# Kernel tuning notes

Measured on AMD Instinct MI355X. Metric: run time of the kernel, lower is better.

## Reference

```python
import jax, jax.numpy as jnp
import numpy as np

B, T, D_IN, H, L, K = 2048, 96, 64, 256, 2, 20


def setup_inputs() -> dict:
    key = jax.random.key(0)
    ks = jax.random.split(key, 16)
    s = 0.05
    b_ih0 = (jax.random.normal(ks[6], (4 * H,)) * s).at[H:2 * H].set(1.0)
    b_hh0 = (jax.random.normal(ks[7], (4 * H,)) * s).at[H:2 * H].set(1.0)
    b_ih1 = (jax.random.normal(ks[8], (4 * H,)) * s).at[H:2 * H].set(1.0)
    b_hh1 = (jax.random.normal(ks[9], (4 * H,)) * s).at[H:2 * H].set(1.0)
    return {
        "train_batch": jax.random.normal(ks[0], (B, T, D_IN), jnp.float32),
        "labels_batch": jax.random.uniform(ks[1], (B, T), jnp.float32),
        "W_ih0": jax.random.normal(ks[2], (4 * H, D_IN)) * s,
        "W_hh0": jax.random.normal(ks[3], (4 * H, H)) * s,
        "W_ih1": jax.random.normal(ks[4], (4 * H, H)) * s,
        "W_hh1": jax.random.normal(ks[5], (4 * H, H)) * s,
        "b_ih0": b_ih0, "b_hh0": b_hh0, "b_ih1": b_ih1, "b_hh1": b_hh1,
        "W_pb": jax.random.normal(ks[10], (1, H * L)) * s,
        "b_pb": jax.random.normal(ks[11], (1,)) * s,
        "W_pg": jax.random.normal(ks[12], (K, H * L)) * s,
        "b_pg": jax.random.normal(ks[13], (K,)) * s,
    }


def _lstm_cell(x, h, c, Wi, Wh, bi, bh):
    z = x @ Wi.T + h @ Wh.T + bi + bh  # [B, 4H]
    i, f, g, o = jnp.split(z, 4, axis=1)
    c2 = jax.nn.sigmoid(f) * c + jax.nn.sigmoid(i) * jnp.tanh(g)
    h2 = jax.nn.sigmoid(o) * jnp.tanh(c2)
    return h2, c2


def _crps_loss(beta0, gamma, y):
    # beta0: [B,1], gamma: [B,K] (both positive via softplus), y: [B]
    k = gamma.shape[1]
    inv_k = 1.0 / k
    # spline quadratic coefficients beta (per knot)
    prev = jnp.concatenate([beta0, gamma[:, :-1]], axis=1)
    b = (gamma - prev) * (0.5 * k)          # (gamma - prev) / (2*sigma)
    b = b - jnp.pad(b, ((0, 0), (1, 0)))[:, :-1]
    b_last = gamma[:, -1] - jnp.sum(b[:, :-1], axis=1)
    b = jnp.concatenate([b[:, :-1], b_last[:, None]], axis=1)  # [B,K]
    ksi_cum = jnp.cumsum(jnp.full_like(gamma, inv_k), axis=1)  # [B,K]
    ksi = jnp.pad(ksi_cum, ((0, 0), (1, 0)))[:, :-1]           # left knots
    # spline CDF value at each interior knot: F(ksi_cum_i)
    kn = jnp.maximum(ksi_cum[:, :, None] - ksi[:, None, :], 0.0)  # [B,K,K]
    F = ksi_cum * beta0 + jnp.sum(kn * kn * b[:, None, :], axis=-1)  # [B,K]
    knots = jnp.pad(F, ((0, 0), (1, 0)))[:, :-1]  # F at left knot of each segment
    diff = y[:, None] - knots                     # [B,K]
    al = diff > 0                                  # active segments
    alf = al.astype(b.dtype)
    A = jnp.sum(alf * b, axis=1)
    Bc = beta0[:, 0] - 2.0 * jnp.sum(alf * b * ksi, axis=1)
    C = -y + jnp.sum(alf * b * ksi * ksi, axis=1)
    disc = Bc * Bc - 4.0 * A * C
    neg_disc = disc < 0
    A_zero = A == 0
    quad_sel = (~A_zero) & (~neg_disc)
    # fallback: alpha = left knot of segment with min |diff|
    amin = jnp.argmin(jnp.abs(diff), axis=1)
    alpha_knot = jnp.take_along_axis(ksi, amin[:, None], axis=1)[:, 0]
    denB = jnp.where(Bc == 0, 1.0, Bc)
    alpha_lin = -C / denB
    disc_safe = jnp.where(quad_sel, disc, 1.0)
    denA = jnp.where(quad_sel, 2.0 * A, 1.0)
    alpha_quad = (-Bc + jnp.sqrt(disc_safe)) / denA
    alpha = jnp.where(quad_sel, alpha_quad,
                      jnp.where(A_zero, alpha_lin, alpha_knot))
    crps1 = -y * (1.0 - 2.0 * alpha)
    crps2 = beta0[:, 0] * (1.0 / 3.0 - alpha * alpha)
    crps3 = jnp.sum(b / 6.0 * (1.0 - ksi) ** 4, axis=1)
    crps4 = jnp.sum(alf * (2.0 / 3.0) * b * (alpha[:, None] - ksi) ** 3, axis=1)
    return jnp.mean(crps1 + crps2 + crps3 - crps4)


def reference(train_batch, labels_batch, W_ih0, W_hh0, W_ih1, W_hh1,
              b_ih0, b_hh0, b_ih1, b_hh1, W_pb, b_pb, W_pg, b_pg):
    xs = jnp.transpose(train_batch, (1, 0, 2))  # [T,B,D]
    ys = labels_batch.T                          # [T,B]
    bsz = train_batch.shape[0]
    h0 = jnp.zeros((bsz, H), train_batch.dtype)
    init = (h0, h0, h0, h0)

    def step(carry, xy):
        h0_, c0_, h1_, c1_ = carry
        x, y = xy
        h0n, c0n = _lstm_cell(x, h0_, c0_, W_ih0, W_hh0, b_ih0, b_hh0)
        h1n, c1n = _lstm_cell(h0n, h1_, c1_, W_ih1, W_hh1, b_ih1, b_hh1)
        # torch: hidden[L,B,H].permute(1,2,0).reshape(B, H*L)
        hp = jnp.stack([h0n, h1n], axis=-1).reshape(x.shape[0], H * L)
        beta0 = jax.nn.softplus(hp @ W_pb.T + b_pb)  # [B,1]
        gamma = jax.nn.softplus(hp @ W_pg.T + b_pg)  # [B,K]
        return (h0n, c0n, h1n, c1n), _crps_loss(beta0, gamma, y)

    _, losses = jax.lax.scan(step, init, (xs, ys))
    return jnp.sum(losses)
```

## Files before the change

### kernel.cpp

```cpp
#include <hip/hip_runtime.h>


typedef __attribute__((ext_vector_type(8))) short short8v;
typedef __attribute__((ext_vector_type(4))) float f32x4;

#define HBUF 524288
#define GSTRIDE 32768

static __device__ __forceinline__ unsigned short f2bf(float f) {
  unsigned int u = __float_as_uint(f);
  u += 0x7fffu + ((u >> 16) & 1u);
  return (unsigned short)(u >> 16);
}
static __device__ __forceinline__ float sigf(float x) { return 1.f / (1.f + __expf(-x)); }
static __device__ __forceinline__ float tanhfast(float x) {
  float xc = fminf(fmaxf(x, -15.f), 15.f);
  float e = __expf(2.f * xc);
  return (e - 1.f) / (e + 1.f);
}
static __device__ __forceinline__ float softplusf(float x) {
  float e = __expf(-fabsf(x));
  float l = __logf(1.f + e);
  return (x > 0.f) ? x + l : l;
}

__global__ void prep_kernel(const float* __restrict__ Wih0, const float* __restrict__ Whh0,
                            const float* __restrict__ Wih1, const float* __restrict__ Whh1,
                            const float* __restrict__ bih0, const float* __restrict__ bhh0,
                            const float* __restrict__ bih1, const float* __restrict__ bhh1,
                            const float* __restrict__ Wpb,  const float* __restrict__ Wpg,
                            unsigned short* __restrict__ W0, unsigned short* __restrict__ W1,
                            unsigned short* __restrict__ Wp,
                            float* __restrict__ bias0, float* __restrict__ bias1) {
  int i = blockIdx.x * 256 + threadIdx.x;
  if (i < 327680) {
    int s = i / 20480, rem = i % 20480;
    int g = rem / 5120, rem2 = rem % 5120;
    int kk = rem2 >> 9, lane = (rem2 >> 3) & 63, e = rem2 & 7;
    int n = g * 256 + s * 16 + (lane & 15);
    int k = kk * 32 + (lane >> 4) * 8 + e;
    float v = (k < 64) ? Wih0[n * 64 + k] : Whh0[n * 256 + (k - 64)];
    W0[i] = f2bf(v);
    return;
  }
  i -= 327680;
  if (i < 524288) {
    int s = i >> 15, rem = i & 32767;
    int g = rem >> 13, rem2 = rem & 8191;
    int kk = rem2 >> 9, lane = (rem2 >> 3) & 63, e = rem2 & 7;
    int n = g * 256 + s * 16 + (lane & 15);
    int k = kk * 32 + (lane >> 4) * 8 + e;
    float v = (k < 256) ? Wih1[n * 256 + k] : Whh1[n * 256 + (k - 256)];
    W1[i] = f2bf(v);
    return;
  }
  i -= 524288;
  if (i < 16384) {
    int nt = i >> 13, rem = i & 8191;
    int kk = rem >> 9, lane = (rem >> 3) & 63, e = rem & 7;
    int o = nt * 16 + (lane & 15);
    int k = kk * 32 + (lane >> 4) * 8 + e;
    int c = (k < 256) ? (2 * k) : (2 * (k - 256) + 1);
    float v = (o == 0) ? Wpb[c] : (o <= 20 ? Wpg[(o - 1) * 512 + c] : 0.f);
    Wp[i] = f2bf(v);
    return;
  }
  i -= 16384;
  if (i < 1024) { bias0[i] = bih0[i] + bhh0[i]; return; }
  i -= 1024;
  if (i < 1024) { bias1[i] = bih1[i] + bhh1[i]; return; }
}

__global__ __launch_bounds__(512, 2) void lstm_crps_kernel(
    const float* __restrict__ X,
    const float* __restrict__ Y,
    const unsigned short* __restrict__ W0f,
    const unsigned short* __restrict__ W1f,
    const unsigned short* __restrict__ WpF,
    const float* __restrict__ bias0, const float* __restrict__ bias1,
    const float* __restrict__ bpb, const float* __restrict__ bpg,
    unsigned short* __restrict__ H0, unsigned short* __restrict__ H1,
    int* __restrict__ flags,
    float* __restrict__ out) {
  __shared__ __align__(16) unsigned short WL0[20480];
  __shared__ __align__(16) unsigned short WL1[32768];
  __shared__ __align__(16) unsigned short WpL[16384];
  __shared__ float PJ[8][22];
  __shared__ float bpgs[20];
  __shared__ float CB[8][24], KN[8][24];

  const int tid = threadIdx.x;
  const int w  = tid >> 6;
  const int l  = tid & 63;
  const int lr = l & 15;
  const int lg = l >> 4;
  const int bid = blockIdx.x;
  const int grp = (bid & 7) * 2 + ((bid >> 3) & 1);
  const int s   = bid >> 4;

  {
    const int4* src0 = (const int4*)(W0f + s * 20480);
    int4* dst0 = (int4*)WL0;
    for (int i = tid; i < 2560; i += 512) dst0[i] = src0[i];
    const int4* src1 = (const int4*)(W1f + s * 32768);
    int4* dst1 = (int4*)WL1;
    for (int i = tid; i < 4096; i += 512) dst1[i] = src1[i];
    const int4* srcp = (const int4*)WpF;
    int4* dstp = (int4*)WpL;
    for (int i = tid; i < 2048; i += 512) dstp[i] = srcp[i];
    if (tid < 20) bpgs[tid] = bpg[tid];
  }

  float bz0[4], bz1[4];
#pragma unroll
  for (int g = 0; g < 4; ++g) {
    int n = g * 256 + 16 * s + lr;
    bz0[g] = bias0[n];
    bz1[g] = bias1[n];
  }
  float c0s[4] = {}, c1s[4] = {};
  float lossacc = 0.f;
  const float bpbv = bpb[0];

  const int myrow = grp * 128 + w * 16 + lr;
  const float* xrowp = X + (size_t)myrow * 96 * 64 + lg * 8;

  __syncthreads();

  for (int it = 0; it <= 96; ++it) {
    const int tA = it - 1;

    short8v h0f[8], h1f[8];
    if (it >= 1) {
      const unsigned short* hp = H0 + (size_t)(tA & 3) * HBUF + (size_t)myrow * 256 + lg * 8;
#pragma unroll
      for (int kk = 0; kk < 8; ++kk) h0f[kk] = *(const short8v*)(hp + kk * 32);
    }
    if (it >= 2) {
      const unsigned short* hp = H1 + (size_t)(it & 1) * HBUF + (size_t)myrow * 256 + lg * 8;
#pragma unroll
      for (int kk = 0; kk < 8; ++kk) h1f[kk] = *(const short8v*)(hp + kk * 32);
    }
    float4 xa0, xa1, xb0, xb1;
    if (it < 96) {
      const float* xp = xrowp + (size_t)it * 64;
      xa0 = *(const float4*)xp;        xa1 = *(const float4*)(xp + 4);
      xb0 = *(const float4*)(xp + 32); xb1 = *(const float4*)(xp + 36);
    }
    float yv = 0.f;
    if (it >= 1 && tid < 8) yv = Y[(size_t)(grp * 128 + 8 * s + tid) * 96 + tA];

    f32x4 acc[4];

    if (it >= 1) {
#pragma unroll
      for (int g = 0; g < 4; ++g) { f32x4 z = {0.f, 0.f, 0.f, 0.f}; acc[g] = z; }
#pragma unroll
      for (int kk = 0; kk < 8; ++kk)
#pragma unroll
        for (int g = 0; g < 4; ++g) {
          short8v b = *(const short8v*)&WL1[((g * 16 + kk) * 64 + l) * 8];
          acc[g] = __builtin_amdgcn_mfma_f32_16x16x32_bf16(h0f[kk], b, acc[g], 0, 0, 0);
        }
      if (it >= 2) {
#pragma unroll
        for (int kk = 0; kk < 8; ++kk)
#pragma unroll
          for (int g = 0; g < 4; ++g) {
            short8v b = *(const short8v*)&WL1[((g * 16 + 8 + kk) * 64 + l) * 8];
            acc[g] = __builtin_amdgcn_mfma_f32_16x16x32_bf16(h1f[kk], b, acc[g], 0, 0, 0);
          }
      }
      unsigned short* h1c = H1 + (size_t)(tA & 1) * HBUF + grp * GSTRIDE;
#pragma unroll
      for (int r = 0; r < 4; ++r) {
        int rowl = w * 16 + lg * 4 + r;
        float cn = sigf(acc[1][r] + bz1[1]) * c1s[r]
                 + sigf(acc[0][r] + bz1[0]) * tanhfast(acc[2][r] + bz1[2]);
        c1s[r] = cn;
        float hn = sigf(acc[3][r] + bz1[3]) * tanhfast(cn);
        h1c[rowl * 256 + 16 * s + lr] = f2bf(hn);
      }
    }

    if (it < 96) {
#pragma unroll
      for (int g = 0; g < 4; ++g) { f32x4 z = {0.f, 0.f, 0.f, 0.f}; acc[g] = z; }
      {
        short8v a0;
        a0[0] = (short)f2bf(xa0.x); a0[1] = (short)f2bf(xa0.y);
        a0[2] = (short)f2bf(xa0.z); a0[3] = (short)f2bf(xa0.w);
        a0[4] = (short)f2bf(xa1.x); a0[5] = (short)f2bf(xa1.y);
        a0[6] = (short)f2bf(xa1.z); a0[7] = (short)f2bf(xa1.w);
#pragma unroll
        for (int g = 0; g < 4; ++g) {
          short8v b = *(const short8v*)&WL0[((g * 10 + 0) * 64 + l) * 8];
          acc[g] = __builtin_amdgcn_mfma_f32_16x16x32_bf16(a0, b, acc[g], 0, 0, 0);
        }
        short8v a1;
        a1[0] = (short)f2bf(xb0.x); a1[1] = (short)f2bf(xb0.y);
        a1[2] = (short)f2bf(xb0.z); a1[3] = (short)f2bf(xb0.w);
        a1[4] = (short)f2bf(xb1.x); a1[5] = (short)f2bf(xb1.y);
        a1[6] = (short)f2bf(xb1.z); a1[7] = (short)f2bf(xb1.w);
#pragma unroll
        for (int g = 0; g < 4; ++g) {
          short8v b = *(const short8v*)&WL0[((g * 10 + 1) * 64 + l) * 8];
          acc[g] = __builtin_amdgcn_mfma_f32_16x16x32_bf16(a1, b, acc[g], 0, 0, 0);
        }
      }
      if (it >= 1) {
#pragma unroll
        for (int kk = 0; kk < 8; ++kk)
#pragma unroll
          for (int g = 0; g < 4; ++g) {
            short8v b = *(const short8v*)&WL0[((g * 10 + 2 + kk) * 64 + l) * 8];
            acc[g] = __builtin_amdgcn_mfma_f32_16x16x32_bf16(h0f[kk], b, acc[g], 0, 0, 0);
          }
      }
      unsigned short* h0c = H0 + (size_t)(it & 3) * HBUF + grp * GSTRIDE;
#pragma unroll
      for (int r = 0; r < 4; ++r) {
        int rowl = w * 16 + lg * 4 + r;
        float cn = sigf(acc[1][r] + bz0[1]) * c0s[r]
                 + sigf(acc[0][r] + bz0[0]) * tanhfast(acc[2][r] + bz0[2]);
        c0s[r] = cn;
        float hn = sigf(acc[3][r] + bz0[3]) * tanhfast(cn);
        h0c[rowl * 256 + 16 * s + lr] = f2bf(hn);
      }
    }

    __syncthreads();
    if (tid == 0) {
      int* f = flags + (it * 16 + grp) * 32;
      __hip_atomic_fetch_add(f, 1, __ATOMIC_RELEASE, __HIP_MEMORY_SCOPE_AGENT);
      while (__hip_atomic_load(f, __ATOMIC_RELAXED, __HIP_MEMORY_SCOPE_AGENT) < 16)
        __builtin_amdgcn_s_sleep(2);
      __builtin_amdgcn_fence(__ATOMIC_ACQUIRE, "agent");
    }
    __syncthreads();

    if (it >= 1) {
      if (w < 2) {
        const int nt = w;
        const size_t prow = (size_t)(grp * 128 + 8 * s + (lr & 7)) * 256 + lg * 8;
        const unsigned short* h0p = H0 + (size_t)(tA & 3) * HBUF + prow;
        const unsigned short* h1p = H1 + (size_t)(tA & 1) * HBUF + prow;
        short8v af[16];
#pragma unroll
        for (int kk = 0; kk < 8; ++kk) af[kk] = *(const short8v*)(h0p + kk * 32);
#pragma unroll
        for (int kk = 0; kk < 8; ++kk) af[8 + kk] = *(const short8v*)(h1p + kk * 32);
        f32x4 ap = {0.f, 0.f, 0.f, 0.f};
#pragma unroll
        for (int kk = 0; kk < 16; ++kk) {
          short8v b = *(const short8v*)&WpL[((nt * 16 + kk) * 64 + l) * 8];
          ap = __builtin_amdgcn_mfma_f32_16x16x32_bf16(af[kk], b, ap, 0, 0, 0);
        }
#pragma unroll
        for (int r = 0; r < 4; ++r) {
          int m = lg * 4 + r, o = nt * 16 + lr;
          if (m < 8 && o < 21)
            PJ[m][o] = ap[r] + ((o == 0) ? bpbv : bpgs[o - 1]);
        }
      }
      __syncthreads();

      if (tid < 8) {
        const int row = tid;
        const float y = yv;
        const float h = 0.05f;
        float beta0 = softplusf(PJ[row][0]);
        {
          float gprev = beta0, brawprev = 0.f, ssum = 0.f, g19 = 0.f;
#pragma unroll
          for (int i2 = 0; i2 < 20; ++i2) {
            float gi = softplusf(PJ[row][1 + i2]);
            float braw = (gi - gprev) * 10.f;
            float bbv = (i2 == 0) ? braw : (braw - brawprev);
            if (i2 < 19) { ssum += bbv; CB[row][i2] = bbv; }
            gprev = gi; brawprev = braw; g19 = gi;
          }
          CB[row][19] = g19 - ssum;
        }
        {
          float S0 = 0.f, S1 = 0.f, S2 = 0.f;
          KN[row][0] = 0.f;
#pragma unroll
          for (int i2 = 0; i2 < 19; ++i2) {
            float bbv = CB[row][i2];
            float fi = (float)i2;
            S0 += bbv; S1 += fi * bbv; S2 += fi * fi * bbv;
            float ip = (float)(i2 + 1);
            KN[row][i2 + 1] = ip * h * beta0 + h * h * (ip * ip * S0 - 2.f * ip * S1 + S2);
          }
        }
        float Aq = 0.f, Bk = 0.f, Ck = 0.f, crps3 = 0.f;
        float best = 1e30f; int amin = 0;
#pragma unroll
        for (int i2 = 0; i2 < 20; ++i2) {
          float knot = KN[row][i2];
          float bbv = CB[row][i2];
          float d = y - knot;
          float ad = fabsf(d);
          if (ad < best) { best = ad; amin = i2; }
          float alf = (d > 0.f) ? 1.f : 0.f;
          float ks = (float)i2 * h;
          float ab = alf * bbv;
          Aq += ab; Bk += ab * ks; Ck += ab * ks * ks;
          float om = 1.f - ks; float om2 = om * om;
          crps3 += bbv * (1.f / 6.f) * om2 * om2;
        }
        float Bc = beta0 - 2.f * Bk;
        float Cc = Ck - y;
        float disc = Bc * Bc - 4.f * Aq * Cc;
        bool az = (Aq == 0.f);
        bool qs = (!az) && (disc >= 0.f);
        float alpha;
        if (qs)      alpha = (-Bc + sqrtf(disc)) / (2.f * Aq);
        else if (az) alpha = -Cc / ((Bc == 0.f) ? 1.f : Bc);
        else         alpha = (float)amin * h;
        float crps4 = 0.f;
#pragma unroll
        for (int i2 = 0; i2 < 20; ++i2) {
          float knot = KN[row][i2];
          float bbv = CB[row][i2];
          float alf = ((y - knot) > 0.f) ? 1.f : 0.f;
          float am = alpha - (float)i2 * h;
          crps4 += alf * (2.f / 3.f) * bbv * am * am * am;
        }
        lossacc += (-y * (1.f - 2.f * alpha) + beta0 * (1.f / 3.f - alpha * alpha)
                    + crps3 - crps4);
      }
    }
  }

  if (w == 0) {
#pragma unroll
    for (int off = 4; off > 0; off >>= 1) lossacc += __shfl_down(lossacc, off, 64);
    if (l == 0) atomicAdd(out, lossacc * (1.f / 2048.f));
  }
}

extern "C" void kernel_launch(void* const* d_in, const int* in_sizes, int n_in,
                              void* d_out, int out_size, void* d_ws, size_t ws_size,
                              hipStream_t stream) {
  const float* X    = (const float*)d_in[0];
  const float* Y    = (const float*)d_in[1];
  const float* Wih0 = (const float*)d_in[2];
  const float* Whh0 = (const float*)d_in[3];
  const float* Wih1 = (const float*)d_in[4];
  const float* Whh1 = (const float*)d_in[5];
  const float* bih0 = (const float*)d_in[6];
  const float* bhh0 = (const float*)d_in[7];
  const float* bih1 = (const float*)d_in[8];
  const float* bhh1 = (const float*)d_in[9];
  const float* Wpb  = (const float*)d_in[10];
  const float* bpb  = (const float*)d_in[11];
  const float* Wpg  = (const float*)d_in[12];
  const float* bpg  = (const float*)d_in[13];

  char* ws = (char*)d_ws;
  unsigned short* W0f = (unsigned short*)(ws);
  unsigned short* W1f = (unsigned short*)(ws + 655360);
  unsigned short* WpF = (unsigned short*)(ws + 1703936);
  float* bias0 = (float*)(ws + 1736704);
  float* bias1 = (float*)(ws + 1740800);
  unsigned short* H0 = (unsigned short*)(ws + 1744896);
  unsigned short* H1 = (unsigned short*)(ws + 5939200);
  int* flags = (int*)(ws + 8036352);

  hipMemsetAsync(d_out, 0, sizeof(float), stream);
  hipMemsetAsync(flags, 0, 198656, stream);
  prep_kernel<<<3400, 256, 0, stream>>>(Wih0, Whh0, Wih1, Whh1, bih0, bhh0, bih1, bhh1,
                                        Wpb, Wpg, W0f, W1f, WpF, bias0, bias1);

  float* outp = (float*)d_out;
  void* kargs[] = {(void*)&X, (void*)&Y, (void*)&W0f, (void*)&W1f, (void*)&WpF,
                   (void*)&bias0, (void*)&bias1, (void*)&bpb, (void*)&bpg,
                   (void*)&H0, (void*)&H1, (void*)&flags, (void*)&outp};
  hipLaunchCooperativeKernel((const void*)lstm_crps_kernel, dim3(256), dim3(512),
                             kargs, 0, stream);
}
```

Baseline: 1.583 ms.

## Have four waves each compute two row tiles, reusing weight fragments across tiles

The LSTM gate GEMMs now run on waves 0-3 only, and each wave handles two 16-row tiles (rows u and u+64). Each weight fragment read from LDS feeds two MFMAs instead of one, halving LDS weight traffic per MFMA and giving more independent MFMA chains. Waves 4 and 5 take over the projection and CRPS work, so it can run on waves that did no gate math. The cost is more registers per wave (double the h fragments and accumulators), now pinned with waves_per_eu(2,2), and half the waves sit idle during the recurrent GEMMs.

```diff
diff --git a/kernel.cpp b/kernel.cpp
--- a/kernel.cpp
+++ b/kernel.cpp
@@ -22,6 +22,14 @@
   float e = __expf(-fabsf(x));
   float l = __logf(1.f + e);
   return (x > 0.f) ? x + l : l;
+}
+static __device__ __forceinline__ short8v pack8(float4 a, float4 b) {
+  short8v r;
+  r[0] = (short)f2bf(a.x); r[1] = (short)f2bf(a.y);
+  r[2] = (short)f2bf(a.z); r[3] = (short)f2bf(a.w);
+  r[4] = (short)f2bf(b.x); r[5] = (short)f2bf(b.y);
+  r[6] = (short)f2bf(b.z); r[7] = (short)f2bf(b.w);
+  return r;
 }
 
 __global__ void prep_kernel(const float* __restrict__ Wih0, const float* __restrict__ Whh0,
@@ -71,7 +79,8 @@
   if (i < 1024) { bias1[i] = bih1[i] + bhh1[i]; return; }
 }
 
-__global__ __launch_bounds__(512, 2) void lstm_crps_kernel(
+__global__ __attribute__((amdgpu_flat_work_group_size(512, 512), amdgpu_waves_per_eu(2, 2)))
+void lstm_crps_kernel(
     const float* __restrict__ X,
     const float* __restrict__ Y,
     const unsigned short* __restrict__ W0f,
@@ -118,114 +127,124 @@
     bz0[g] = bias0[n];
     bz1[g] = bias1[n];
   }
-  float c0s[4] = {}, c1s[4] = {};
+  float c0s[2][4] = {}, c1s[2][4] = {};
   float lossacc = 0.f;
   const float bpbv = bpb[0];
 
-  const int myrow = grp * 128 + w * 16 + lr;
-  const float* xrowp = X + (size_t)myrow * 96 * 64 + lg * 8;
+  const int u = w & 3;
+  const size_t rA = (size_t)(grp * 128 + u * 16 + lr);
+  const size_t rB = rA + 64;
+  const float* xpA = X + rA * 96 * 64 + lg * 8;
+  const float* xpB = X + rB * 96 * 64 + lg * 8;
 
   __syncthreads();
 
   for (int it = 0; it <= 96; ++it) {
     const int tA = it - 1;
 
-    short8v h0f[8], h1f[8];
-    if (it >= 1) {
-      const unsigned short* hp = H0 + (size_t)(tA & 3) * HBUF + (size_t)myrow * 256 + lg * 8;
-#pragma unroll
-      for (int kk = 0; kk < 8; ++kk) h0f[kk] = *(const short8v*)(hp + kk * 32);
-    }
-    if (it >= 2) {
-      const unsigned short* hp = H1 + (size_t)(it & 1) * HBUF + (size_t)myrow * 256 + lg * 8;
-#pragma unroll
-      for (int kk = 0; kk < 8; ++kk) h1f[kk] = *(const short8v*)(hp + kk * 32);
-    }
-    float4 xa0, xa1, xb0, xb1;
-    if (it < 96) {
-      const float* xp = xrowp + (size_t)it * 64;
-      xa0 = *(const float4*)xp;        xa1 = *(const float4*)(xp + 4);
-      xb0 = *(const float4*)(xp + 32); xb1 = *(const float4*)(xp + 36);
-    }
     float yv = 0.f;
-    if (it >= 1 && tid < 8) yv = Y[(size_t)(grp * 128 + 8 * s + tid) * 96 + tA];
-
-    f32x4 acc[4];
-
-    if (it >= 1) {
-#pragma unroll
-      for (int g = 0; g < 4; ++g) { f32x4 z = {0.f, 0.f, 0.f, 0.f}; acc[g] = z; }
-#pragma unroll
-      for (int kk = 0; kk < 8; ++kk)
-#pragma unroll
-        for (int g = 0; g < 4; ++g) {
-          short8v b = *(const short8v*)&WL1[((g * 16 + kk) * 64 + l) * 8];
-          acc[g] = __builtin_amdgcn_mfma_f32_16x16x32_bf16(h0f[kk], b, acc[g], 0, 0, 0);
-        }
+    if (it >= 1 && w == 4 && l < 8) yv = Y[(size_t)(grp * 128 + 8 * s + l) * 96 + tA];
+
+    if (w < 4) {
+      short8v h0A[8], h0B[8], h1A[8], h1B[8];
+      if (it >= 1) {
+        const unsigned short* pa = H0 + (size_t)(tA & 3) * HBUF + rA * 256 + lg * 8;
+        const unsigned short* pb = H0 + (size_t)(tA & 3) * HBUF + rB * 256 + lg * 8;
+#pragma unroll
+        for (int kk = 0; kk < 8; ++kk) { h0A[kk] = *(const short8v*)(pa + kk * 32);
+                                         h0B[kk] = *(const short8v*)(pb + kk * 32); }
+      }
       if (it >= 2) {
+        const unsigned short* pa = H1 + (size_t)(it & 1) * HBUF + rA * 256 + lg * 8;
+        const unsigned short* pb = H1 + (size_t)(it & 1) * HBUF + rB * 256 + lg * 8;
+#pragma unroll
+        for (int kk = 0; kk < 8; ++kk) { h1A[kk] = *(const short8v*)(pa + kk * 32);
+                                         h1B[kk] = *(const short8v*)(pb + kk * 32); }
+      }
+      short8v xfA[2], xfB[2];
+      if (it < 96) {
+        const float* xp = xpA + (size_t)it * 64;
+        xfA[0] = pack8(*(const float4*)xp, *(const float4*)(xp + 4));
+        xfA[1] = pack8(*(const float4*)(xp + 32), *(const float4*)(xp + 36));
+        const float* xq = xpB + (size_t)it * 64;
+        xfB[0] = pack8(*(const float4*)xq, *(const float4*)(xq + 4));
+        xfB[1] = pack8(*(const float4*)(xq + 32), *(const float4*)(xq + 36));
+      }
+
+      f32x4 acc[2][4];
+
+      if (it >= 1) {
+#pragma unroll
+        for (int m = 0; m < 2; ++m)
+#pragma unroll
+          for (int g = 0; g < 4; ++g) { f32x4 z = {0.f, 0.f, 0.f, 0.f}; acc[m][g] = z; }
 #pragma unroll
         for (int kk = 0; kk < 8; ++kk)
 #pragma unroll
           for (int g = 0; g < 4; ++g) {
-            short8v b = *(const short8v*)&WL1[((g * 16 + 8 + kk) * 64 + l) * 8];
-            acc[g] = __builtin_amdgcn_mfma_f32_16x16x32_bf16(h1f[kk], b, acc[g], 0, 0, 0);
-          }
-      }
-      unsigned short* h1c = H1 + (size_t)(tA & 1) * HBUF + grp * GSTRIDE;
-#pragma unroll
-      for (int r = 0; r < 4; ++r) {
-        int rowl = w * 16 + lg * 4 + r;
-        float cn = sigf(acc[1][r] + bz1[1]) * c1s[r]
-                 + sigf(acc[0][r] + bz1[0]) * tanhfast(acc[2][r] + bz1[2]);
-        c1s[r] = cn;
-        float hn = sigf(acc[3][r] + bz1[3]) * tanhfast(cn);
-        h1c[rowl * 256 + 16 * s + lr] = f2bf(hn);
-      }
-    }
-
-    if (it < 96) {
-#pragma unroll
-      for (int g = 0; g < 4; ++g) { f32x4 z = {0.f, 0.f, 0.f, 0.f}; acc[g] = z; }
-      {
-        short8v a0;
-        a0[0] = (short)f2bf(xa0.x); a0[1] = (short)f2bf(xa0.y);
-        a0[2] = (short)f2bf(xa0.z); a0[3] = (short)f2bf(xa0.w);
-        a0[4] = (short)f2bf(xa1.x); a0[5] = (short)f2bf(xa1.y);
-        a0[6] = (short)f2bf(xa1.z); a0[7] = (short)f2bf(xa1.w);
-#pragma unroll
-        for (int g = 0; g < 4; ++g) {
-          short8v b = *(const short8v*)&WL0[((g * 10 + 0) * 64 + l) * 8];
-          acc[g] = __builtin_amdgcn_mfma_f32_16x16x32_bf16(a0, b, acc[g], 0, 0, 0);
-        }
-        short8v a1;
-        a1[0] = (short)f2bf(xb0.x); a1[1] = (short)f2bf(xb0.y);
-        a1[2] = (short)f2bf(xb0.z); a1[3] = (short)f2bf(xb0.w);
-        a1[4] = (short)f2bf(xb1.x); a1[5] = (short)f2bf(xb1.y);
-        a1[6] = (short)f2bf(xb1.z); a1[7] = (short)f2bf(xb1.w);
-#pragma unroll
-        for (int g = 0; g < 4; ++g) {
-          short8v b = *(const short8v*)&WL0[((g * 10 + 1) * 64 + l) * 8];
-          acc[g] = __builtin_amdgcn_mfma_f32_16x16x32_bf16(a1, b, acc[g], 0, 0, 0);
-        }
-      }
-      if (it >= 1) {
-#pragma unroll
-        for (int kk = 0; kk < 8; ++kk)
+            short8v b = *(const short8v*)&WL1[((g * 16 + kk) * 64 + l) * 8];
+            acc[0][g] = __builtin_amdgcn_mfma_f32_16x16x32_bf16(h0A[kk], b, acc[0][g], 0, 0, 0);
+            acc[1][g] = __builtin_amdgcn_mfma_f32_16x16x32_bf16(h0B[kk], b, acc[1][g], 0, 0, 0);
+          }
+        if (it >= 2) {
+#pragma unroll
+          for (int kk = 0; kk < 8; ++kk)
+#pragma unroll
+            for (int g = 0; g < 4; ++g) {
+              short8v b = *(const short8v*)&WL1[((g * 16 + 8 + kk) * 64 + l) * 8];
+              acc[0][g] = __builtin_amdgcn_mfma_f32_16x16x32_bf16(h1A[kk], b, acc[0][g], 0, 0, 0);
+              acc[1][g] = __builtin_amdgcn_mfma_f32_16x16x32_bf16(h1B[kk], b, acc[1][g], 0, 0, 0);
+            }
+        }
+        unsigned short* h1c = H1 + (size_t)(tA & 1) * HBUF + grp * GSTRIDE;
+#pragma unroll
+        for (int m = 0; m < 2; ++m)
+#pragma unroll
+          for (int r = 0; r < 4; ++r) {
+            int rowl = (u + 4 * m) * 16 + lg * 4 + r;
+            float cn = sigf(acc[m][1][r] + bz1[1]) * c1s[m][r]
+                     + sigf(acc[m][0][r] + bz1[0]) * tanhfast(acc[m][2][r] + bz1[2]);
+            c1s[m][r] = cn;
+            float hn = sigf(acc[m][3][r] + bz1[3]) * tanhfast(cn);
+            h1c[rowl * 256 + 16 * s + lr] = f2bf(hn);
+          }
+      }
+
+      if (it < 96) {
+#pragma unroll
+        for (int m = 0; m < 2; ++m)
+#pragma unroll
+          for (int g = 0; g < 4; ++g) { f32x4 z = {0.f, 0.f, 0.f, 0.f}; acc[m][g] = z; }
+#pragma unroll
+        for (int kk = 0; kk < 2; ++kk)
 #pragma unroll
           for (int g = 0; g < 4; ++g) {
-            short8v b = *(const short8v*)&WL0[((g * 10 + 2 + kk) * 64 + l) * 8];
-            acc[g] = __builtin_amdgcn_mfma_f32_16x16x32_bf16(h0f[kk], b, acc[g], 0, 0, 0);
-          }
-      }
-      unsigned short* h0c = H0 + (size_t)(it & 3) * HBUF + grp * GSTRIDE;
-#pragma unroll
-      for (int r = 0; r < 4; ++r) {
-        int rowl = w * 16 + lg * 4 + r;
-        float cn = sigf(acc[1][r] + bz0[1]) * c0s[r]
-                 + sigf(acc[0][r] + bz0[0]) * tanhfast(acc[2][r] + bz0[2]);
-        c0s[r] = cn;
-        float hn = sigf(acc[3][r] + bz0[3]) * tanhfast(cn);
-        h0c[rowl * 256 + 16 * s + lr] = f2bf(hn);
+            short8v b = *(const short8v*)&WL0[((g * 10 + kk) * 64 + l) * 8];
+            acc[0][g] = __builtin_amdgcn_mfma_f32_16x16x32_bf16(xfA[kk], b, acc[0][g], 0, 0, 0);
+            acc[1][g] = __builtin_amdgcn_mfma_f32_16x16x32_bf16(xfB[kk], b, acc[1][g], 0, 0, 0);
+          }
+        if (it >= 1) {
+#pragma unroll
+          for (int kk = 0; kk < 8; ++kk)
+#pragma unroll
+            for (int g = 0; g < 4; ++g) {
+              short8v b = *(const short8v*)&WL0[((g * 10 + 2 + kk) * 64 + l) * 8];
+              acc[0][g] = __builtin_amdgcn_mfma_f32_16x16x32_bf16(h0A[kk], b, acc[0][g], 0, 0, 0);
+              acc[1][g] = __builtin_amdgcn_mfma_f32_16x16x32_bf16(h0B[kk], b, acc[1][g], 0, 0, 0);
+            }
+        }
+        unsigned short* h0c = H0 + (size_t)(it & 3) * HBUF + grp * GSTRIDE;
+#pragma unroll
+        for (int m = 0; m < 2; ++m)
+#pragma unroll
+          for (int r = 0; r < 4; ++r) {
+            int rowl = (u + 4 * m) * 16 + lg * 4 + r;
+            float cn = sigf(acc[m][1][r] + bz0[1]) * c0s[m][r]
+                     + sigf(acc[m][0][r] + bz0[0]) * tanhfast(acc[m][2][r] + bz0[2]);
+            c0s[m][r] = cn;
+            float hn = sigf(acc[m][3][r] + bz0[3]) * tanhfast(cn);
+            h0c[rowl * 256 + 16 * s + lr] = f2bf(hn);
+          }
       }
     }
 
@@ -240,8 +259,8 @@
     __syncthreads();
 
     if (it >= 1) {
-      if (w < 2) {
-        const int nt = w;
+      if (w == 4 || w == 5) {
+        const int nt = w & 1;
         const size_t prow = (size_t)(grp * 128 + 8 * s + (lr & 7)) * 256 + lg * 8;
         const unsigned short* h0p = H0 + (size_t)(tA & 3) * HBUF + prow;
         const unsigned short* h1p = H1 + (size_t)(tA & 1) * HBUF + prow;
@@ -265,8 +284,8 @@
       }
       __syncthreads();
 
-      if (tid < 8) {
-        const int row = tid;
+      if (w == 4 && l < 8) {
+        const int row = l;
         const float y = yv;
         const float h = 0.05f;
         float beta0 = softplusf(PJ[row][0]);
@@ -334,7 +353,7 @@
     }
   }
 
-  if (w == 0) {
+  if (w == 4) {
 #pragma unroll
     for (int off = 4; off > 0; off >>= 1) lossacc += __shfl_down(lossacc, off, 64);
     if (l == 0) atomicAdd(out, lossacc * (1.f / 2048.f));
```

Result: slower. 2.360 ms (+49.1%).
